# Kernel tuning notes

Measured on AMD Instinct MI355X. Metric: run time of the kernel, lower is better.

## Reference

```python
import jax, jax.numpy as jnp
import numpy as np

B, N, C, K = 4, 4096, 64, 32   # graphs, points/graph, feat dim, max_neighbors
R = 0.2                         # radius
H1, H2, H3 = 64, 64, 128        # edge-MLP widths (nn = MLP([C+3, 64, 64, 128]))


def setup_inputs() -> dict:
    key = jax.random.key(0)
    ks = jax.random.split(key, 6)
    x = jax.random.normal(ks[0], (B * N, C), jnp.float32)
    pos = jax.random.uniform(ks[1], (B * N, 3), jnp.float32)  # unit cube
    batch = jnp.repeat(jnp.arange(B, dtype=jnp.int32), N)      # sorted, equal-size graphs
    W1 = jax.random.normal(ks[2], (C + 3, H1), jnp.float32) * 0.1
    b1 = jnp.zeros((H1,), jnp.float32)
    W2 = jax.random.normal(ks[3], (H1, H2), jnp.float32) * 0.1
    b2 = jnp.zeros((H2,), jnp.float32)
    W3 = jax.random.normal(ks[4], (H2, H3), jnp.float32) * 0.1
    b3 = jnp.zeros((H3,), jnp.float32)
    return dict(x=x, pos=pos, batch=batch, W1=W1, b1=b1, W2=W2, b2=b2, W3=W3, b3=b3)


def reference(x, pos, batch, W1, b1, W2, b2, W3, b3):
    # ratio == 1.0 -> idx = all points (identity sampling per the torch code).
    posb = pos.reshape(B, N, 3)
    xb = x.reshape(B, N, C)

    # radius neighbor search within each graph: squared pairwise distances [B, N_tgt, N_src]
    p2 = jnp.sum(posb * posb, axis=-1)                              # [B,N]
    d2 = p2[:, :, None] + p2[:, None, :] - 2.0 * jnp.einsum('bnd,bmd->bnm', posb, posb)
    score = jnp.where(d2 <= R * R, -d2, -jnp.inf)                   # valid -> nearest-first
    top, nb = jax.lax.top_k(score, K)                               # [B,N,K] K nearest in ball
    valid = jnp.isfinite(top)                                        # self (d2=0) always valid -> covers add_self_loops

    gather = jax.vmap(lambda arr, idx: arr[idx])                     # per-graph gather
    x_j = gather(xb, nb)                                             # [B,N,K,C]
    pos_j = gather(posb, nb)                                         # [B,N,K,3]
    rel = pos_j - posb[:, :, None, :]                                # pos_j - pos_i

    # PointNetConv message: h = nn([x_j, pos_j - pos_i]); nn = Lin+ReLU x3
    h = jnp.concatenate([x_j, rel], axis=-1)                         # [B,N,K,C+3]
    h = jax.nn.relu(h @ W1 + b1)
    h = jax.nn.relu(h @ W2 + b2)
    h = jax.nn.relu(h @ W3 + b3)                                     # [B,N,K,H3]

    # max aggregation over neighbors (PointNetConv default aggr='max')
    neg = jnp.finfo(h.dtype).min
    h = jnp.where(valid[..., None], h, neg)
    out = jnp.max(h, axis=2).reshape(B * N, H3)                      # [B*N, 128]

    return out, pos, batch
```

## Files before the change

### kernel.cpp

```cpp
#include <hip/hip_runtime.h>
#include <hip/hip_bf16.h>
#include <float.h>
#include <stdint.h>

#define NPTS 4096
#define NB_K 32
#define CAP  256

typedef short bf16x8 __attribute__((ext_vector_type(8)));
typedef float f32x4  __attribute__((ext_vector_type(4)));
#define MFMA_BF16 __builtin_amdgcn_mfma_f32_16x16x32_bf16
#define SCHED_FENCE() __builtin_amdgcn_sched_barrier(0)

__device__ __forceinline__ short bf16rne(float f) {
    unsigned u = __float_as_uint(f);
    unsigned r = u + 0x7fffu + ((u >> 16) & 1u);
    return (short)(r >> 16);
}
__device__ __forceinline__ short bfc(float f) {
    __hip_bfloat16 h = __float2bfloat16(f);
    return __builtin_bit_cast(short, h);
}

__global__ __launch_bounds__(256) void wprep_kernel(const float* __restrict__ W1,
                                                    const float* __restrict__ W2,
                                                    const float* __restrict__ W3,
                                                    short* __restrict__ frg) {
    const int t = threadIdx.x + blockIdx.x * 256;
    if (t >= 36 * 64) return;
    const int frag = t >> 6, lane = t & 63;
    const int col16 = lane & 15, kg = lane >> 4;
    bf16x8 v;
    if (frag < 12) {
        const int s = frag >> 2, n = frag & 3;
        #pragma unroll
        for (int j = 0; j < 8; ++j) {
            const int k = s * 32 + kg * 8 + j;
            v[j] = (k < 67) ? bf16rne(W1[k * 64 + n * 16 + col16]) : (short)0;
        }
    } else if (frag < 20) {
        const int s = (frag - 12) >> 2, n = (frag - 12) & 3;
        #pragma unroll
        for (int j = 0; j < 8; ++j) {
            const int k = (2 * s + (j >> 2)) * 16 + kg * 4 + (j & 3);
            v[j] = bf16rne(W2[k * 64 + n * 16 + col16]);
        }
    } else {
        const int s = (frag - 20) >> 3, n = (frag - 20) & 7;
        #pragma unroll
        for (int j = 0; j < 8; ++j) {
            const int k = (2 * s + (j >> 2)) * 16 + kg * 4 + (j & 3);
            v[j] = bf16rne(W3[k * 128 + n * 16 + col16]);
        }
    }
    *(bf16x8*)(frg + (size_t)t * 8) = v;
}

__global__ __launch_bounds__(256, 4) void knn_kernel(const float* __restrict__ pos,
                                                     unsigned short* __restrict__ nb16) {
    __shared__ int cand[8][CAP];
    const int tid = threadIdx.x;
    const int wv = tid >> 6, lane = tid & 63;
    const int tgtA = (blockIdx.x * 4 + wv) * 2;
    const int gb = tgtA & ~(NPTS - 1);
    const unsigned long long ltm = (1ull << lane) - 1ull;

    const float tAx = pos[(size_t)tgtA * 3 + 0];
    const float tAy = pos[(size_t)tgtA * 3 + 1];
    const float tAz = pos[(size_t)tgtA * 3 + 2];
    const float tBx = pos[(size_t)(tgtA + 1) * 3 + 0];
    const float tBy = pos[(size_t)(tgtA + 1) * 3 + 1];
    const float tBz = pos[(size_t)(tgtA + 1) * 3 + 2];
    const float RFILT = 0.040001f;

    int cntA = 0, cntB = 0;
    for (int c0 = 0; c0 < NPTS; c0 += 64) {
        const int j = c0 + lane;
        const float* pp = pos + (size_t)(gb + j) * 3;
        const float px = pp[0], py = pp[1], pz = pp[2];
        {
            const float dx = px - tAx, dy = py - tAy, dz = pz - tAz;
            const float d2 = fmaf(dx, dx, fmaf(dy, dy, dz * dz));
            const bool want = d2 <= RFILT;
            const unsigned long long m = __ballot(want);
            const int wp = cntA + __popcll(m & ltm);
            if (want && wp < CAP) cand[wv * 2][wp] = j;
            cntA += __popcll(m);
        }
        {
            const float dx = px - tBx, dy = py - tBy, dz = pz - tBz;
            const float d2 = fmaf(dx, dx, fmaf(dy, dy, dz * dz));
            const bool want = d2 <= RFILT;
            const unsigned long long m = __ballot(want);
            const int wp = cntB + __popcll(m & ltm);
            if (want && wp < CAP) cand[wv * 2 + 1][wp] = j;
            cntB += __popcll(m);
        }
    }
    if (cntA > CAP) cntA = CAP;
    if (cntB > CAP) cntB = CAP;

    const double RR = 0.2 * 0.2;
    const unsigned long long INF = ~0ull;

    for (int t = 0; t < 2; ++t) {
        const int tgt = tgtA + t;
        const int cnt = t ? cntB : cntA;
        const int* cd = cand[wv * 2 + t];
        const double txd = (double)pos[(size_t)tgt * 3 + 0];
        const double tyd = (double)pos[(size_t)tgt * 3 + 1];
        const double tzd = (double)pos[(size_t)tgt * 3 + 2];

        unsigned long long k0 = INF, k1 = INF, k2 = INF, k3 = INF;
#define LOADK(KS, S)                                                          \
        { const int p = lane + 64 * (S);                                      \
          if (p < cnt) {                                                      \
              const int ci = cd[p];                                           \
              const float* cp = pos + (size_t)(gb + ci) * 3;                  \
              const double ddx = (double)cp[0] - txd;                         \
              const double ddy = (double)cp[1] - tyd;                         \
              const double ddz = (double)cp[2] - tzd;                         \
              const double dd = fma(ddx, ddx, fma(ddy, ddy, ddz * ddz));      \
              if (dd <= RR)                                                   \
                  KS = ((unsigned long long)__double_as_longlong(dd)          \
                        & ~0xfffULL) | (unsigned long long)ci;                \
          } }
        LOADK(k0, 0) LOADK(k1, 1) LOADK(k2, 2) LOADK(k3, 3)
#undef LOADK

        const int cnt2 = __popcll(__ballot(k0 != INF)) + __popcll(__ballot(k1 != INF))
                       + __popcll(__ballot(k2 != INF)) + __popcll(__ballot(k3 != INF));

        unsigned long long pivot = 0xFFFFFFFFFFFFFFFEull;
        if (cnt2 > NB_K) {
            unsigned long long lo = 0, hi = 0x3FA5000000000000ull;
            for (int it = 0; it < 70; ++it) {
                const unsigned long long mid = lo + ((hi - lo) >> 1);
                const int c = __popcll(__ballot(k0 <= mid)) + __popcll(__ballot(k1 <= mid))
                            + __popcll(__ballot(k2 <= mid)) + __popcll(__ballot(k3 <= mid));
                if (c == NB_K) { pivot = mid; break; }
                if (c < NB_K) lo = mid + 1; else hi = mid - 1;
            }
        }

        int base = 0;
#define EMIT(KS)                                                              \
        { const bool sel = (KS <= pivot);                                     \
          const unsigned long long m = __ballot(sel);                         \
          const int wp = base + __popcll(m & ltm);                            \
          if (sel && wp < NB_K)                                               \
              nb16[(size_t)tgt * NB_K + wp] = (unsigned short)(KS & 0xfff);   \
          base += __popcll(m); }
        EMIT(k0) EMIT(k1) EMIT(k2) EMIT(k3)
#undef EMIT
        if (lane >= base && lane < NB_K)
            nb16[(size_t)tgt * NB_K + lane] = (unsigned short)0xFFFF;
    }
}

__global__ __launch_bounds__(256, 4) void mlp_kernel(
    const float* __restrict__ x, const float* __restrict__ pos, const int* __restrict__ batch,
    const float* __restrict__ b1, const float* __restrict__ b2, const float* __restrict__ b3,
    const unsigned short* __restrict__ nb16, const short* __restrict__ frg,
    float* __restrict__ out) {
    __shared__ short bfr[36 * 64 * 8];

    const int tid = threadIdx.x, wv = tid >> 6, lane = tid & 63;

    for (int i = tid; i < 36 * 64; i += 256)
        *(bf16x8*)(bfr + (size_t)i * 8) = *(const bf16x8*)(frg + (size_t)i * 8);
    __syncthreads();

    const int c0 = lane & 15, kg = lane >> 4, rlow = kg * 4;
    const int wbase = blockIdx.x * 4 + wv;
    const int gb = (wbase * 4) & ~(NPTS - 1);

    int nvAll[2];
    #pragma unroll
    for (int q = 0; q < 2; ++q)
        nvAll[q] = (int)nb16[(size_t)(wbase * 4 + q * 2 + (lane >> 5)) * 32 + (lane & 31)];

    for (int p = 0; p < 4; ++p) {
        const int tgt = wbase * 4 + p;
        const int nv = nvAll[p >> 1];
        const unsigned long long bm = __ballot(nv != 0xFFFF);
        const unsigned vmask = (p & 1) ? (unsigned)(bm >> 32) : (unsigned)bm;

        int jrow[2];
        #pragma unroll
        for (int mm = 0; mm < 2; ++mm) {
            const int j = __shfl(nv, (p & 1) * 32 + mm * 16 + c0);
            jrow[mm] = (j == 0xFFFF) ? 0 : j;
        }

        bf16x8 X1[2][3];
        #pragma unroll
        for (int mm = 0; mm < 2; ++mm) {
            const float* xr = x + (size_t)(gb + jrow[mm]) * 64;
            #pragma unroll
            for (int s = 0; s < 2; ++s) {
                const float4* p4 = (const float4*)(xr + s * 32 + kg * 8);
                const float4 u = p4[0], w = p4[1];
                bf16x8 a;
                a[0] = bfc(u.x); a[1] = bfc(u.y); a[2] = bfc(u.z); a[3] = bfc(u.w);
                a[4] = bfc(w.x); a[5] = bfc(w.y); a[6] = bfc(w.z); a[7] = bfc(w.w);
                X1[mm][s] = a;
            }
            bf16x8 a = {0, 0, 0, 0, 0, 0, 0, 0};
            if (kg == 0) {
                const float* pj = pos + (size_t)(gb + jrow[mm]) * 3;
                const float* pi = pos + (size_t)tgt * 3;
                a[0] = bfc(pj[0] - pi[0]);
                a[1] = bfc(pj[1] - pi[1]);
                a[2] = bfc(pj[2] - pi[2]);
            }
            X1[mm][2] = a;
        }

        bf16x8 B2[2][2];
        #pragma unroll
        for (int nt = 0; nt < 4; ++nt) {
            const float4 bb = *(const float4*)(b1 + nt * 16 + rlow);
            f32x4 acc[2];
            acc[0] = acc[1] = f32x4{bb.x, bb.y, bb.z, bb.w};
            #pragma unroll
            for (int s = 0; s < 3; ++s) {
                const bf16x8 Wf = *(const bf16x8*)(bfr + (size_t)((s * 4 + nt) * 64 + lane) * 8);
                #pragma unroll
                for (int mm = 0; mm < 2; ++mm)
                    acc[mm] = MFMA_BF16(Wf, X1[mm][s], acc[mm], 0, 0, 0);
            }
            #pragma unroll
            for (int mm = 0; mm < 2; ++mm)
                #pragma unroll
                for (int r = 0; r < 4; ++r)
                    B2[mm][nt >> 1][(nt & 1) * 4 + r] = bfc(fmaxf(acc[mm][r], 0.f));
            SCHED_FENCE();
        }

        bf16x8 A3[2][2];
        #pragma unroll
        for (int nt = 0; nt < 4; ++nt) {
            const float4 bb = *(const float4*)(b2 + nt * 16 + rlow);
            f32x4 acc[2];
            acc[0] = acc[1] = f32x4{bb.x, bb.y, bb.z, bb.w};
            #pragma unroll
            for (int s = 0; s < 2; ++s) {
                const bf16x8 Wf = *(const bf16x8*)(bfr + (size_t)((12 + s * 4 + nt) * 64 + lane) * 8);
                #pragma unroll
                for (int mm = 0; mm < 2; ++mm)
                    acc[mm] = MFMA_BF16(Wf, B2[mm][s], acc[mm], 0, 0, 0);
            }
            #pragma unroll
            for (int mm = 0; mm < 2; ++mm)
                #pragma unroll
                for (int r = 0; r < 4; ++r)
                    A3[mm][nt >> 1][(nt & 1) * 4 + r] = bfc(fmaxf(acc[mm][r], 0.f));
            SCHED_FENCE();
        }

        #pragma unroll
        for (int n = 0; n < 8; ++n) {
            const float bv = b3[n * 16 + c0];
            f32x4 acc[2];
            acc[0] = acc[1] = f32x4{bv, bv, bv, bv};
            #pragma unroll
            for (int s = 0; s < 2; ++s) {
                const bf16x8 Bf = *(const bf16x8*)(bfr + (size_t)((20 + s * 8 + n) * 64 + lane) * 8);
                #pragma unroll
                for (int mm = 0; mm < 2; ++mm)
                    acc[mm] = MFMA_BF16(A3[mm][s], Bf, acc[mm], 0, 0, 0);
            }
            float v = 0.f;
            #pragma unroll
            for (int mm = 0; mm < 2; ++mm)
                #pragma unroll
                for (int r = 0; r < 4; ++r) {
                    const int row = mm * 16 + rlow + r;
                    const float h = fmaxf(acc[mm][r], 0.f);
                    v = fmaxf(v, ((vmask >> row) & 1u) ? h : 0.f);
                }
            v = fmaxf(v, __shfl_xor(v, 16));
            v = fmaxf(v, __shfl_xor(v, 32));
            if (lane < 16) out[(size_t)tgt * 128 + n * 16 + lane] = v;
            SCHED_FENCE();
        }

        if (lane < 3)  out[2097152 + (size_t)tgt * 3 + lane] = pos[(size_t)tgt * 3 + lane];
        if (lane == 3) out[2146304 + tgt] = (float)batch[tgt];
    }
}

extern "C" void kernel_launch(void* const* d_in, const int* in_sizes, int n_in,
                              void* d_out, int out_size, void* d_ws, size_t ws_size,
                              hipStream_t stream) {
    const float* x   = (const float*)d_in[0];
    const float* pos = (const float*)d_in[1];
    const int* batch = (const int*)d_in[2];
    const float* W1  = (const float*)d_in[3];
    const float* b1  = (const float*)d_in[4];
    const float* W2  = (const float*)d_in[5];
    const float* b2  = (const float*)d_in[6];
    const float* W3  = (const float*)d_in[7];
    const float* b3  = (const float*)d_in[8];
    float* out = (float*)d_out;

    unsigned short* nb16 = (unsigned short*)d_ws;
    short* frg = (short*)((char*)d_ws + (1 << 20));

    hipLaunchKernelGGL(wprep_kernel, dim3(9), dim3(256), 0, stream, W1, W2, W3, frg);
    hipLaunchKernelGGL(knn_kernel, dim3(2048), dim3(256), 0, stream, pos, nb16);
    hipLaunchKernelGGL(mlp_kernel, dim3(1024), dim3(256), 0, stream,
                       x, pos, batch, b1, b2, b3, nb16, frg, out);
}
```

Baseline: 86.91 us.

## Fuse neighbor search and edge MLP into one kernel sharing LDS via union

Merges the radius kNN kernel and the MLP kernel into a single launch, where each block finds neighbors for 8 targets and keeps the neighbor lists in LDS instead of writing them to global memory. The candidate buffer and the weight-fragment buffer share LDS through a union, separated by a barrier. This removes one kernel launch and the global round trip for neighbor indices. In exchange each block now reloads all weight fragments for only 8 targets instead of 16, and each wave handles 2 targets instead of 4 in the MLP phase.

```diff
diff --git a/kernel.cpp b/kernel.cpp
--- a/kernel.cpp
+++ b/kernel.cpp
@@ -56,140 +56,138 @@
     *(bf16x8*)(frg + (size_t)t * 8) = v;
 }
 
-__global__ __launch_bounds__(256, 4) void knn_kernel(const float* __restrict__ pos,
-                                                     unsigned short* __restrict__ nb16) {
-    __shared__ int cand[8][CAP];
+__global__ __launch_bounds__(256, 4) void fused_kernel(
+    const float* __restrict__ x, const float* __restrict__ pos, const int* __restrict__ batch,
+    const float* __restrict__ b1, const float* __restrict__ b2, const float* __restrict__ b3,
+    const short* __restrict__ frg, float* __restrict__ out) {
+    __shared__ union {
+        struct {
+            int cand[8][CAP];
+            unsigned short nbl[8][32];
+        } p1;
+        short bfr[36 * 64 * 8];
+    } lds;
+
     const int tid = threadIdx.x;
     const int wv = tid >> 6, lane = tid & 63;
-    const int tgtA = (blockIdx.x * 4 + wv) * 2;
+    const unsigned long long ltm = (1ull << lane) - 1ull;
+
+    const int tgtA = blockIdx.x * 8 + wv * 2;
     const int gb = tgtA & ~(NPTS - 1);
-    const unsigned long long ltm = (1ull << lane) - 1ull;
-
-    const float tAx = pos[(size_t)tgtA * 3 + 0];
-    const float tAy = pos[(size_t)tgtA * 3 + 1];
-    const float tAz = pos[(size_t)tgtA * 3 + 2];
-    const float tBx = pos[(size_t)(tgtA + 1) * 3 + 0];
-    const float tBy = pos[(size_t)(tgtA + 1) * 3 + 1];
-    const float tBz = pos[(size_t)(tgtA + 1) * 3 + 2];
-    const float RFILT = 0.040001f;
-
-    int cntA = 0, cntB = 0;
-    for (int c0 = 0; c0 < NPTS; c0 += 64) {
-        const int j = c0 + lane;
-        const float* pp = pos + (size_t)(gb + j) * 3;
-        const float px = pp[0], py = pp[1], pz = pp[2];
-        {
-            const float dx = px - tAx, dy = py - tAy, dz = pz - tAz;
-            const float d2 = fmaf(dx, dx, fmaf(dy, dy, dz * dz));
-            const bool want = d2 <= RFILT;
-            const unsigned long long m = __ballot(want);
-            const int wp = cntA + __popcll(m & ltm);
-            if (want && wp < CAP) cand[wv * 2][wp] = j;
-            cntA += __popcll(m);
-        }
-        {
-            const float dx = px - tBx, dy = py - tBy, dz = pz - tBz;
-            const float d2 = fmaf(dx, dx, fmaf(dy, dy, dz * dz));
-            const bool want = d2 <= RFILT;
-            const unsigned long long m = __ballot(want);
-            const int wp = cntB + __popcll(m & ltm);
-            if (want && wp < CAP) cand[wv * 2 + 1][wp] = j;
-            cntB += __popcll(m);
+
+    {
+        const float tAx = pos[(size_t)tgtA * 3 + 0];
+        const float tAy = pos[(size_t)tgtA * 3 + 1];
+        const float tAz = pos[(size_t)tgtA * 3 + 2];
+        const float tBx = pos[(size_t)(tgtA + 1) * 3 + 0];
+        const float tBy = pos[(size_t)(tgtA + 1) * 3 + 1];
+        const float tBz = pos[(size_t)(tgtA + 1) * 3 + 2];
+        const float RFILT = 0.040001f;
+
+        int cntA = 0, cntB = 0;
+        for (int c0 = 0; c0 < NPTS; c0 += 64) {
+            const int j = c0 + lane;
+            const float* pp = pos + (size_t)(gb + j) * 3;
+            const float px = pp[0], py = pp[1], pz = pp[2];
+            {
+                const float dx = px - tAx, dy = py - tAy, dz = pz - tAz;
+                const float d2 = fmaf(dx, dx, fmaf(dy, dy, dz * dz));
+                const bool want = d2 <= RFILT;
+                const unsigned long long m = __ballot(want);
+                const int wp = cntA + __popcll(m & ltm);
+                if (want && wp < CAP) lds.p1.cand[wv * 2][wp] = j;
+                cntA += __popcll(m);
+            }
+            {
+                const float dx = px - tBx, dy = py - tBy, dz = pz - tBz;
+                const float d2 = fmaf(dx, dx, fmaf(dy, dy, dz * dz));
+                const bool want = d2 <= RFILT;
+                const unsigned long long m = __ballot(want);
+                const int wp = cntB + __popcll(m & ltm);
+                if (want && wp < CAP) lds.p1.cand[wv * 2 + 1][wp] = j;
+                cntB += __popcll(m);
+            }
+        }
+        if (cntA > CAP) cntA = CAP;
+        if (cntB > CAP) cntB = CAP;
+
+        const double RR = 0.2 * 0.2;
+        const unsigned long long INF = ~0ull;
+
+        for (int t = 0; t < 2; ++t) {
+            const int tgt = tgtA + t;
+            const int cnt = t ? cntB : cntA;
+            const int* cd = lds.p1.cand[wv * 2 + t];
+            const double txd = (double)pos[(size_t)tgt * 3 + 0];
+            const double tyd = (double)pos[(size_t)tgt * 3 + 1];
+            const double tzd = (double)pos[(size_t)tgt * 3 + 2];
+
+            unsigned long long k0 = INF, k1 = INF, k2 = INF, k3 = INF;
+#define LOADK(KS, S)                                                          \
+            { const int p = lane + 64 * (S);                                  \
+              if (p < cnt) {                                                  \
+                  const int ci = cd[p];                                       \
+                  const float* cp = pos + (size_t)(gb + ci) * 3;              \
+                  const double ddx = (double)cp[0] - txd;                     \
+                  const double ddy = (double)cp[1] - tyd;                     \
+                  const double ddz = (double)cp[2] - tzd;                     \
+                  const double dd = fma(ddx, ddx, fma(ddy, ddy, ddz * ddz));  \
+                  if (dd <= RR)                                               \
+                      KS = ((unsigned long long)__double_as_longlong(dd)      \
+                            & ~0xfffULL) | (unsigned long long)ci;            \
+              } }
+            LOADK(k0, 0) LOADK(k1, 1) LOADK(k2, 2) LOADK(k3, 3)
+#undef LOADK
+
+            const int cnt2 = __popcll(__ballot(k0 != INF)) + __popcll(__ballot(k1 != INF))
+                           + __popcll(__ballot(k2 != INF)) + __popcll(__ballot(k3 != INF));
+
+            unsigned long long pivot = 0xFFFFFFFFFFFFFFFEull;
+            if (cnt2 > NB_K) {
+                unsigned long long lo = 0, hi = 0x3FA5000000000000ull;
+                for (int it = 0; it < 70; ++it) {
+                    const unsigned long long mid = lo + ((hi - lo) >> 1);
+                    const int c = __popcll(__ballot(k0 <= mid)) + __popcll(__ballot(k1 <= mid))
+                                + __popcll(__ballot(k2 <= mid)) + __popcll(__ballot(k3 <= mid));
+                    if (c == NB_K) { pivot = mid; break; }
+                    if (c < NB_K) lo = mid + 1; else hi = mid - 1;
+                }
+            }
+
+            int base = 0;
+#define EMIT(KS)                                                              \
+            { const bool sel = (KS <= pivot);                                 \
+              const unsigned long long m = __ballot(sel);                     \
+              const int wp = base + __popcll(m & ltm);                        \
+              if (sel && wp < NB_K)                                           \
+                  lds.p1.nbl[wv * 2 + t][wp] = (unsigned short)(KS & 0xfff);  \
+              base += __popcll(m); }
+            EMIT(k0) EMIT(k1) EMIT(k2) EMIT(k3)
+#undef EMIT
+            if (lane >= base && lane < NB_K)
+                lds.p1.nbl[wv * 2 + t][lane] = (unsigned short)0xFFFF;
         }
     }
-    if (cntA > CAP) cntA = CAP;
-    if (cntB > CAP) cntB = CAP;
-
-    const double RR = 0.2 * 0.2;
-    const unsigned long long INF = ~0ull;
-
-    for (int t = 0; t < 2; ++t) {
-        const int tgt = tgtA + t;
-        const int cnt = t ? cntB : cntA;
-        const int* cd = cand[wv * 2 + t];
-        const double txd = (double)pos[(size_t)tgt * 3 + 0];
-        const double tyd = (double)pos[(size_t)tgt * 3 + 1];
-        const double tzd = (double)pos[(size_t)tgt * 3 + 2];
-
-        unsigned long long k0 = INF, k1 = INF, k2 = INF, k3 = INF;
-#define LOADK(KS, S)                                                          \
-        { const int p = lane + 64 * (S);                                      \
-          if (p < cnt) {                                                      \
-              const int ci = cd[p];                                           \
-              const float* cp = pos + (size_t)(gb + ci) * 3;                  \
-              const double ddx = (double)cp[0] - txd;                         \
-              const double ddy = (double)cp[1] - tyd;                         \
-              const double ddz = (double)cp[2] - tzd;                         \
-              const double dd = fma(ddx, ddx, fma(ddy, ddy, ddz * ddz));      \
-              if (dd <= RR)                                                   \
-                  KS = ((unsigned long long)__double_as_longlong(dd)          \
-                        & ~0xfffULL) | (unsigned long long)ci;                \
-          } }
-        LOADK(k0, 0) LOADK(k1, 1) LOADK(k2, 2) LOADK(k3, 3)
-#undef LOADK
-
-        const int cnt2 = __popcll(__ballot(k0 != INF)) + __popcll(__ballot(k1 != INF))
-                       + __popcll(__ballot(k2 != INF)) + __popcll(__ballot(k3 != INF));
-
-        unsigned long long pivot = 0xFFFFFFFFFFFFFFFEull;
-        if (cnt2 > NB_K) {
-            unsigned long long lo = 0, hi = 0x3FA5000000000000ull;
-            for (int it = 0; it < 70; ++it) {
-                const unsigned long long mid = lo + ((hi - lo) >> 1);
-                const int c = __popcll(__ballot(k0 <= mid)) + __popcll(__ballot(k1 <= mid))
-                            + __popcll(__ballot(k2 <= mid)) + __popcll(__ballot(k3 <= mid));
-                if (c == NB_K) { pivot = mid; break; }
-                if (c < NB_K) lo = mid + 1; else hi = mid - 1;
-            }
-        }
-
-        int base = 0;
-#define EMIT(KS)                                                              \
-        { const bool sel = (KS <= pivot);                                     \
-          const unsigned long long m = __ballot(sel);                         \
-          const int wp = base + __popcll(m & ltm);                            \
-          if (sel && wp < NB_K)                                               \
-              nb16[(size_t)tgt * NB_K + wp] = (unsigned short)(KS & 0xfff);   \
-          base += __popcll(m); }
-        EMIT(k0) EMIT(k1) EMIT(k2) EMIT(k3)
-#undef EMIT
-        if (lane >= base && lane < NB_K)
-            nb16[(size_t)tgt * NB_K + lane] = (unsigned short)0xFFFF;
-    }
-}
-
-__global__ __launch_bounds__(256, 4) void mlp_kernel(
-    const float* __restrict__ x, const float* __restrict__ pos, const int* __restrict__ batch,
-    const float* __restrict__ b1, const float* __restrict__ b2, const float* __restrict__ b3,
-    const unsigned short* __restrict__ nb16, const short* __restrict__ frg,
-    float* __restrict__ out) {
-    __shared__ short bfr[36 * 64 * 8];
-
-    const int tid = threadIdx.x, wv = tid >> 6, lane = tid & 63;
+
+    const int nv = (int)lds.p1.nbl[wv * 2 + (lane >> 5)][lane & 31];
+
+    __syncthreads();
 
     for (int i = tid; i < 36 * 64; i += 256)
-        *(bf16x8*)(bfr + (size_t)i * 8) = *(const bf16x8*)(frg + (size_t)i * 8);
+        *(bf16x8*)(lds.bfr + (size_t)i * 8) = *(const bf16x8*)(frg + (size_t)i * 8);
     __syncthreads();
 
     const int c0 = lane & 15, kg = lane >> 4, rlow = kg * 4;
-    const int wbase = blockIdx.x * 4 + wv;
-    const int gb = (wbase * 4) & ~(NPTS - 1);
-
-    int nvAll[2];
-    #pragma unroll
-    for (int q = 0; q < 2; ++q)
-        nvAll[q] = (int)nb16[(size_t)(wbase * 4 + q * 2 + (lane >> 5)) * 32 + (lane & 31)];
-
-    for (int p = 0; p < 4; ++p) {
-        const int tgt = wbase * 4 + p;
-        const int nv = nvAll[p >> 1];
-        const unsigned long long bm = __ballot(nv != 0xFFFF);
-        const unsigned vmask = (p & 1) ? (unsigned)(bm >> 32) : (unsigned)bm;
+    const unsigned long long bm = __ballot(nv != 0xFFFF);
+
+    for (int p = 0; p < 2; ++p) {
+        const int tgt = tgtA + p;
+        const unsigned vmask = p ? (unsigned)(bm >> 32) : (unsigned)bm;
 
         int jrow[2];
         #pragma unroll
         for (int mm = 0; mm < 2; ++mm) {
-            const int j = __shfl(nv, (p & 1) * 32 + mm * 16 + c0);
+            const int j = __shfl(nv, p * 32 + mm * 16 + c0);
             jrow[mm] = (j == 0xFFFF) ? 0 : j;
         }
 
@@ -225,7 +223,7 @@
             acc[0] = acc[1] = f32x4{bb.x, bb.y, bb.z, bb.w};
             #pragma unroll
             for (int s = 0; s < 3; ++s) {
-                const bf16x8 Wf = *(const bf16x8*)(bfr + (size_t)((s * 4 + nt) * 64 + lane) * 8);
+                const bf16x8 Wf = *(const bf16x8*)(lds.bfr + (size_t)((s * 4 + nt) * 64 + lane) * 8);
                 #pragma unroll
                 for (int mm = 0; mm < 2; ++mm)
                     acc[mm] = MFMA_BF16(Wf, X1[mm][s], acc[mm], 0, 0, 0);
@@ -246,7 +244,7 @@
             acc[0] = acc[1] = f32x4{bb.x, bb.y, bb.z, bb.w};
             #pragma unroll
             for (int s = 0; s < 2; ++s) {
-                const bf16x8 Wf = *(const bf16x8*)(bfr + (size_t)((12 + s * 4 + nt) * 64 + lane) * 8);
+                const bf16x8 Wf = *(const bf16x8*)(lds.bfr + (size_t)((12 + s * 4 + nt) * 64 + lane) * 8);
                 #pragma unroll
                 for (int mm = 0; mm < 2; ++mm)
                     acc[mm] = MFMA_BF16(Wf, B2[mm][s], acc[mm], 0, 0, 0);
@@ -266,7 +264,7 @@
             acc[0] = acc[1] = f32x4{bv, bv, bv, bv};
             #pragma unroll
             for (int s = 0; s < 2; ++s) {
-                const bf16x8 Bf = *(const bf16x8*)(bfr + (size_t)((20 + s * 8 + n) * 64 + lane) * 8);
+                const bf16x8 Bf = *(const bf16x8*)(lds.bfr + (size_t)((20 + s * 8 + n) * 64 + lane) * 8);
                 #pragma unroll
                 for (int mm = 0; mm < 2; ++mm)
                     acc[mm] = MFMA_BF16(A3[mm][s], Bf, acc[mm], 0, 0, 0);
@@ -305,11 +303,9 @@
     const float* b3  = (const float*)d_in[8];
     float* out = (float*)d_out;
 
-    unsigned short* nb16 = (unsigned short*)d_ws;
     short* frg = (short*)((char*)d_ws + (1 << 20));
 
     hipLaunchKernelGGL(wprep_kernel, dim3(9), dim3(256), 0, stream, W1, W2, W3, frg);
-    hipLaunchKernelGGL(knn_kernel, dim3(2048), dim3(256), 0, stream, pos, nb16);
-    hipLaunchKernelGGL(mlp_kernel, dim3(1024), dim3(256), 0, stream,
-                       x, pos, batch, b1, b2, b3, nb16, frg, out);
-}
+    hipLaunchKernelGGL(fused_kernel, dim3(2048), dim3(256), 0, stream,
+                       x, pos, batch, b1, b2, b3, frg, out);
+}
```

After: 116.5 us. 1.34x slower.

## Fold weight prep and x-to-bf16 conversion into knn kernel, feed bf16 x to MLP

Applied to the files above, without the earlier changes.

Removes the separate weight-prep launch by running it in the first nine blocks of the knn kernel. The knn kernel also converts all of x to bf16 into the workspace, so the MLP kernel gathers half-size rows with no per-edge conversion. This saves one launch and cuts gather traffic in the MLP. In exchange, knn does an extra streaming pass over x, and the workspace layout is shifted.

```diff
diff --git a/kernel.cpp b/kernel.cpp
--- a/kernel.cpp
+++ b/kernel.cpp
@@ -22,44 +22,50 @@
     return __builtin_bit_cast(short, h);
 }
 
-__global__ __launch_bounds__(256) void wprep_kernel(const float* __restrict__ W1,
-                                                    const float* __restrict__ W2,
-                                                    const float* __restrict__ W3,
-                                                    short* __restrict__ frg) {
-    const int t = threadIdx.x + blockIdx.x * 256;
-    if (t >= 36 * 64) return;
-    const int frag = t >> 6, lane = t & 63;
-    const int col16 = lane & 15, kg = lane >> 4;
-    bf16x8 v;
-    if (frag < 12) {
-        const int s = frag >> 2, n = frag & 3;
-        #pragma unroll
-        for (int j = 0; j < 8; ++j) {
-            const int k = s * 32 + kg * 8 + j;
-            v[j] = (k < 67) ? bf16rne(W1[k * 64 + n * 16 + col16]) : (short)0;
-        }
-    } else if (frag < 20) {
-        const int s = (frag - 12) >> 2, n = (frag - 12) & 3;
-        #pragma unroll
-        for (int j = 0; j < 8; ++j) {
-            const int k = (2 * s + (j >> 2)) * 16 + kg * 4 + (j & 3);
-            v[j] = bf16rne(W2[k * 64 + n * 16 + col16]);
-        }
-    } else {
-        const int s = (frag - 20) >> 3, n = (frag - 20) & 7;
-        #pragma unroll
-        for (int j = 0; j < 8; ++j) {
-            const int k = (2 * s + (j >> 2)) * 16 + kg * 4 + (j & 3);
-            v[j] = bf16rne(W3[k * 128 + n * 16 + col16]);
-        }
-    }
-    *(bf16x8*)(frg + (size_t)t * 8) = v;
-}
-
-__global__ __launch_bounds__(256, 4) void knn_kernel(const float* __restrict__ pos,
-                                                     unsigned short* __restrict__ nb16) {
+__global__ __launch_bounds__(256, 4) void knn_kernel(
+    const float* __restrict__ x, const float* __restrict__ pos,
+    const float* __restrict__ W1, const float* __restrict__ W2, const float* __restrict__ W3,
+    unsigned short* __restrict__ nb16, short* __restrict__ frg, short* __restrict__ xb) {
     __shared__ int cand[8][CAP];
     const int tid = threadIdx.x;
+
+    {
+        const size_t base = ((size_t)blockIdx.x * 256 + tid) * 2;
+        const float2 f = *(const float2*)(x + base);
+        short2 o; o.x = bfc(f.x); o.y = bfc(f.y);
+        *(short2*)(xb + base) = o;
+    }
+
+    if (blockIdx.x < 9) {
+        const int t = blockIdx.x * 256 + tid;
+        const int frag = t >> 6, lane = t & 63;
+        const int col16 = lane & 15, kg = lane >> 4;
+        bf16x8 v;
+        if (frag < 12) {
+            const int s = frag >> 2, n = frag & 3;
+            #pragma unroll
+            for (int j = 0; j < 8; ++j) {
+                const int k = s * 32 + kg * 8 + j;
+                v[j] = (k < 67) ? bf16rne(W1[k * 64 + n * 16 + col16]) : (short)0;
+            }
+        } else if (frag < 20) {
+            const int s = (frag - 12) >> 2, n = (frag - 12) & 3;
+            #pragma unroll
+            for (int j = 0; j < 8; ++j) {
+                const int k = (2 * s + (j >> 2)) * 16 + kg * 4 + (j & 3);
+                v[j] = bf16rne(W2[k * 64 + n * 16 + col16]);
+            }
+        } else {
+            const int s = (frag - 20) >> 3, n = (frag - 20) & 7;
+            #pragma unroll
+            for (int j = 0; j < 8; ++j) {
+                const int k = (2 * s + (j >> 2)) * 16 + kg * 4 + (j & 3);
+                v[j] = bf16rne(W3[k * 128 + n * 16 + col16]);
+            }
+        }
+        *(bf16x8*)(frg + (size_t)t * 8) = v;
+    }
+
     const int wv = tid >> 6, lane = tid & 63;
     const int tgtA = (blockIdx.x * 4 + wv) * 2;
     const int gb = tgtA & ~(NPTS - 1);
@@ -159,7 +165,7 @@
 }
 
 __global__ __launch_bounds__(256, 4) void mlp_kernel(
-    const float* __restrict__ x, const float* __restrict__ pos, const int* __restrict__ batch,
+    const short* __restrict__ xb, const float* __restrict__ pos, const int* __restrict__ batch,
     const float* __restrict__ b1, const float* __restrict__ b2, const float* __restrict__ b3,
     const unsigned short* __restrict__ nb16, const short* __restrict__ frg,
     float* __restrict__ out) {
@@ -196,16 +202,10 @@
         bf16x8 X1[2][3];
         #pragma unroll
         for (int mm = 0; mm < 2; ++mm) {
-            const float* xr = x + (size_t)(gb + jrow[mm]) * 64;
-            #pragma unroll
-            for (int s = 0; s < 2; ++s) {
-                const float4* p4 = (const float4*)(xr + s * 32 + kg * 8);
-                const float4 u = p4[0], w = p4[1];
-                bf16x8 a;
-                a[0] = bfc(u.x); a[1] = bfc(u.y); a[2] = bfc(u.z); a[3] = bfc(u.w);
-                a[4] = bfc(w.x); a[5] = bfc(w.y); a[6] = bfc(w.z); a[7] = bfc(w.w);
-                X1[mm][s] = a;
-            }
+            const short* xr = xb + (size_t)(gb + jrow[mm]) * 64;
+            #pragma unroll
+            for (int s = 0; s < 2; ++s)
+                X1[mm][s] = *(const bf16x8*)(xr + s * 32 + kg * 8);
             bf16x8 a = {0, 0, 0, 0, 0, 0, 0, 0};
             if (kg == 0) {
                 const float* pj = pos + (size_t)(gb + jrow[mm]) * 3;
@@ -305,11 +305,12 @@
     const float* b3  = (const float*)d_in[8];
     float* out = (float*)d_out;
 
-    unsigned short* nb16 = (unsigned short*)d_ws;
-    short* frg = (short*)((char*)d_ws + (1 << 20));
-
-    hipLaunchKernelGGL(wprep_kernel, dim3(9), dim3(256), 0, stream, W1, W2, W3, frg);
-    hipLaunchKernelGGL(knn_kernel, dim3(2048), dim3(256), 0, stream, pos, nb16);
+    short* xb = (short*)d_ws;
+    unsigned short* nb16 = (unsigned short*)((char*)d_ws + (2 << 20));
+    short* frg = (short*)((char*)d_ws + (3 << 20));
+
+    hipLaunchKernelGGL(knn_kernel, dim3(2048), dim3(256), 0, stream,
+                       x, pos, W1, W2, W3, nb16, frg, xb);
     hipLaunchKernelGGL(mlp_kernel, dim3(1024), dim3(256), 0, stream,
-                       x, pos, batch, b1, b2, b3, nb16, frg, out);
-}
+                       xb, pos, batch, b1, b2, b3, nb16, frg, out);
+}
```

Result: faster. 77.55 us (median of 2 runs) (-10.8%).
